# Performance work log

Measured on AMD Instinct MI355X. Metric: run time of the kernel, lower is better.

Reference implementation:

```python
import jax, jax.numpy as jnp
import numpy as np

B, N, T, CIN = 16, 400, 12, 2
HID, H, D = 256, 8, 32
P, EMB, TOPK, K = 3, 10, 16, 3


def _conv1d(x, w, b, dil):
    # x: (BN, C, T), w: (O, I, K); causal (left) padding like F.pad((pad,0))
    pad = (K - 1) * dil
    y = jax.lax.conv_general_dilated(x, w, (1,), [(pad, 0)], rhs_dilation=(dil,),
                                     dimension_numbers=('NCH', 'OIH', 'NCH'))
    return y + b[None, :, None]


def _ln(x, g, b):
    m = x.mean(-1, keepdims=True)
    v = x.var(-1, keepdims=True)
    return (x - m) / jnp.sqrt(v + 1e-5) * g + b


def setup_inputs() -> dict:
    key = jax.random.key(0)
    kit = iter(jax.random.split(key, 64))

    def g(shape, s=0.05):
        return jax.random.normal(next(kit), shape, jnp.float32) * s

    # fixed graph: ring with 8 neighbors + self loop -> L = 9*N edges
    idx = np.arange(N)
    offs = np.array([-4, -3, -2, -1, 0, 1, 2, 3, 4])
    recv = np.repeat(idx, offs.size)
    send = (recv + np.tile(offs, N)) % N
    L = recv.size

    inp = {
        'x': g((B, N, T, CIN), 1.0),
        'edge_feat': g((B, L, 2), 1.0),
        'fixed_edge_index': jnp.asarray(np.stack([recv, send]).astype(np.int32)),
        # GTCN layer 0 (dilation 1): gate/filter/skip convs + LayerNorm
        'wg0': g((HID, CIN, K)), 'bg0': jnp.zeros((HID,), jnp.float32),
        'wf0': g((HID, CIN, K)), 'bf0': jnp.zeros((HID,), jnp.float32),
        'ws0': g((HID, CIN, K)), 'bs0': jnp.zeros((HID,), jnp.float32),
        'ln0g': jnp.ones((HID,), jnp.float32), 'ln0b': jnp.zeros((HID,), jnp.float32),
        # GTCN layer 1 (dilation 2)
        'wg1': g((HID, HID, K)), 'bg1': jnp.zeros((HID,), jnp.float32),
        'wf1': g((HID, HID, K)), 'bf1': jnp.zeros((HID,), jnp.float32),
        'ws1': g((HID, HID, K)), 'bs1': jnp.zeros((HID,), jnp.float32),
        'ln1g': jnp.ones((HID,), jnp.float32), 'ln1b': jnp.zeros((HID,), jnp.float32),
        'wsk': g((CIN, HID)), 'bsk': jnp.zeros((HID,), jnp.float32),
        # sparse GAT on fixed physical graph (with 2-dim edge features)
        'sWq': g((HID, HID)), 'sWk': g((HID, HID)), 'sWv': g((HID, HID)),
        'sWe': g((2, HID)),
        'saq': g((H, D)), 'sak': g((H, D)), 'sae': g((H, D)),
        # dense GAT on adaptive adjacency
        'dWq': g((HID, HID)), 'dWk': g((HID, HID)), 'dWv': g((HID, HID)),
        'daq': g((H, D)), 'dak': g((H, D)),
        'E1': g((N, EMB), 0.5), 'E2': g((N, EMB), 0.5),
        # gated fusion
        'fW1': g((HID, HID)), 'fb1': jnp.zeros((HID,), jnp.float32),
        'fW2': g((HID, HID)), 'fb2': jnp.zeros((HID,), jnp.float32),
        'fW3': g((HID, HID)), 'fb3': jnp.zeros((HID,), jnp.float32),
        # prediction head
        'Wo': g((HID, P)), 'bo': jnp.zeros((P,), jnp.float32),
    }
    return inp


def reference(x, edge_feat,
              wg0, bg0, wf0, bf0, ws0, bs0, ln0g, ln0b,
              wg1, bg1, wf1, bf1, ws1, bs1, ln1g, ln1b, wsk, bsk,
              sWq, sWk, sWv, sWe, saq, sak, sae,
              dWq, dWk, dWv, daq, dak, E1, E2,
              fW1, fb1, fW2, fb2, fW3, fb3, Wo, bo,
              fixed_edge_index):
    Bb, Nn, Tt, _ = x.shape
    # ---- GTCN (gated temporal conv stack with residual skip) ----
    res = x @ wsk + bsk                                   # (B,N,T,HID)
    xc = x.reshape(Bb * Nn, Tt, -1).transpose(0, 2, 1)    # (BN,C,T)
    for (wg, bg, wf, bf, ws, bs, lg, lb), dil in (
            ((wg0, bg0, wf0, bf0, ws0, bs0, ln0g, ln0b), 1),
            ((wg1, bg1, wf1, bf1, ws1, bs1, ln1g, ln1b), 2)):
        gate = jax.nn.sigmoid(_conv1d(xc, wg, bg, dil))
        y = gate * _conv1d(xc, wf, bf, dil) + (1 - gate) * _conv1d(xc, ws, bs, dil)
        y = jax.nn.relu(_ln(y.transpose(0, 2, 1), lg, lb))  # (BN,T,HID)
        xc = y.transpose(0, 2, 1)
    h = xc.transpose(0, 2, 1).reshape(Bb, Nn, Tt, HID) + res
    hl = h[:, :, -1, :]                                   # (B,N,HID) last step

    # ---- sparse GAT on fixed physical graph (edge features) ----
    recv, send = fixed_edge_index[0], fixed_edge_index[1]
    q = (hl @ sWq).reshape(Bb, Nn, H, D)
    k = (hl @ sWk).reshape(Bb, Nn, H, D)
    v = (hl @ sWv).reshape(Bb, Nn, H, D)
    e = (edge_feat @ sWe).reshape(Bb, -1, H, D)
    s = (q[:, recv] * saq).sum(-1) + (k[:, send] * sak).sum(-1) + (e * sae).sum(-1)
    s = jax.nn.leaky_relu(s, 0.2)                         # (B,L,H)
    mx = jnp.full((Bb, Nn, H), -jnp.inf, s.dtype).at[:, recv].max(s)
    ex = jnp.exp(s - mx[:, recv])
    den = jnp.zeros((Bb, Nn, H), s.dtype).at[:, recv].add(ex)
    alpha = ex / jnp.clip(den[:, recv], 1e-12, None)
    agg = jnp.zeros((Bb, Nn, H, D), v.dtype).at[:, recv].add(alpha[..., None] * v[:, send])
    h_fixed = jax.nn.elu(agg.reshape(Bb, Nn, HID))

    # ---- dense GAT on adaptive (learned, top-k sparsified) adjacency ----
    A = jax.nn.softmax(jax.nn.relu(E1 @ E2.T), axis=-1)   # (N,N)
    kth = jax.lax.top_k(A, TOPK)[0][:, -1:]
    adj_adp = jnp.where(A >= kth, A, 0.0)
    q = (hl @ dWq).reshape(Bb, Nn, H, D)
    k = (hl @ dWk).reshape(Bb, Nn, H, D)
    v = (hl @ dWv).reshape(Bb, Nn, H, D)
    sc = (q * daq).sum(-1)[:, :, None, :] + (k * dak).sum(-1)[:, None, :, :]  # (B,N,N,H)
    sc = jax.nn.leaky_relu(sc, 0.2)
    sc = sc + jnp.log(jnp.clip(adj_adp, 1e-12, None))[None, :, :, None]      # log-adj trick
    sc = jnp.where((adj_adp > 0)[None, :, :, None], sc, -1e9)
    al = jax.nn.softmax(sc, axis=2)
    h_adp = jax.nn.elu(jnp.einsum('bnjh,bjhd->bnhd', al, v).reshape(Bb, Nn, HID))

    # ---- gated fusion + prediction head ----
    gate = jax.nn.sigmoid((h_fixed + h_adp) @ fW1 + fb1)
    fused = jnp.tanh(gate * (h_fixed @ fW2 + fb2) + (1 - gate) * (h_adp @ fW3 + fb3))
    return fused @ Wo + bo                                # (B,N,P)
```

## Files before the change

kernel.cpp:

```cpp
#include <hip/hip_runtime.h>
#include <math.h>

#define LL 3600
#define NODES 6400

typedef __attribute__((ext_vector_type(8))) _Float16 half8;
typedef __attribute__((ext_vector_type(4))) float f32x4;

__device__ __forceinline__ unsigned short f2h(float f) {
    union { _Float16 h; unsigned short u; } cv;
    cv.h = (_Float16)f;
    return cv.u;
}
__device__ __forceinline__ float h2f(unsigned short u) {
    union { unsigned short u; _Float16 h; } cv;
    cv.u = u;
    return (float)cv.h;
}

#define GLOAD16(gp, lp) __builtin_amdgcn_global_load_lds( \
    (const __attribute__((address_space(1))) unsigned int*)(const void*)(gp), \
    (__attribute__((address_space(3))) unsigned int*)(void*)(lp), 16, 0, 0)

__device__ __forceinline__ void block_reduce_sum2(float a, float b, float* red, float& ra, float& rb) {
    #pragma unroll
    for (int o = 32; o > 0; o >>= 1) { a += __shfl_xor(a, o, 64); b += __shfl_xor(b, o, 64); }
    int w = threadIdx.x >> 6, l = threadIdx.x & 63;
    if (l == 0) { red[w] = a; red[4 + w] = b; }
    __syncthreads();
    ra = red[0] + red[1] + red[2] + red[3];
    rb = red[4] + red[5] + red[6] + red[7];
    __syncthreads();
}

__global__ __launch_bounds__(256) void prep_kernel(
    const float* __restrict__ wg1, const float* __restrict__ wf1, const float* __restrict__ ws1,
    const float* __restrict__ sWv, const float* __restrict__ dWv,
    const float* __restrict__ sWq, const float* __restrict__ saq,
    const float* __restrict__ sWk, const float* __restrict__ sak,
    const float* __restrict__ dWq, const float* __restrict__ daq,
    const float* __restrict__ dWk, const float* __restrict__ dak,
    const float* __restrict__ fW1, const float* __restrict__ fW2, const float* __restrict__ fW3,
    const float* __restrict__ sWe, const float* __restrict__ sae,
    const float* __restrict__ E1, const float* __restrict__ E2,
    const float* __restrict__ x,
    const float* __restrict__ wg0, const float* __restrict__ bg0,
    const float* __restrict__ wf0, const float* __restrict__ bf0,
    const float* __restrict__ ws0, const float* __restrict__ bs0,
    const float* __restrict__ lg0, const float* __restrict__ lb0,
    unsigned short* __restrict__ W1h,
    unsigned short* __restrict__ W2h,
    unsigned short* __restrict__ W3h,
    float* __restrict__ AeS,
    int* __restrict__ cnt, int* __restrict__ idxs, float* __restrict__ logv,
    unsigned short* __restrict__ Xh) {
    __shared__ float smem[22];
    int bid = blockIdx.x;
    int tid = threadIdx.x;

    if (bid < 2304) {
        int idx = bid * 256 + tid;
        int n = idx / 768, k = idx % 768;
        int which = n >> 8, o = n & 255;
        int tt = k >> 8, i = k & 255;
        const float* w = which == 0 ? wg1 : (which == 1 ? wf1 : ws1);
        W1h[idx] = f2h(w[(o * 256 + i) * 3 + tt]);
    } else if (bid < 2944) {
        int idx = (bid - 2304) * 256 + tid;
        int n = idx / 256, k = idx % 256;
        float v = 0.f;
        if (n < 256) v = sWv[k * 256 + n];
        else if (n < 512) v = dWv[k * 256 + (n - 256)];
        else if (n < 544) {
            int j = n - 512, g = j >> 3, h = j & 7;
            const float* Wm = g == 0 ? sWq : (g == 1 ? sWk : (g == 2 ? dWq : dWk));
            const float* am = g == 0 ? saq : (g == 1 ? sak : (g == 2 ? daq : dak));
            float s = 0.f;
            for (int d = 0; d < 32; d++) s += Wm[k * 256 + h * 32 + d] * am[h * 32 + d];
            v = s;
        }
        W2h[idx] = f2h(v);
    } else if (bid < 4480) {
        int idx = (bid - 2944) * 256 + tid;
        int n = idx / 512, k = idx % 512;
        float v = 0.f;
        if (k < 256) {
            if (n < 256) v = fW1[k * 256 + n];
            else if (n < 512) v = fW2[k * 256 + (n - 256)];
        } else {
            int c = k - 256;
            if (n < 256) v = fW1[c * 256 + n];
            else if (n >= 512) v = fW3[c * 256 + (n - 512)];
        }
        W3h[idx] = f2h(v);
    } else if (bid == 4480) {
        if (tid < 16) {
            int cc = tid / 8, h = tid % 8;
            float s = 0.f;
            for (int d = 0; d < 32; d++) s += sWe[cc * 256 + h * 32 + d] * sae[h * 32 + d];
            AeS[tid] = s;
        }
    } else if (bid < 4581) {
        int n = ((bid - 4481) * 256 + tid) >> 6;
        int lane = tid & 63;
        if (n >= 400) return;
        float e1[10];
        #pragma unroll
        for (int k = 0; k < 10; k++) e1[k] = E1[n * 10 + k];
        float p[7];
        #pragma unroll
        for (int i = 0; i < 7; i++) {
            int j = i * 64 + lane;
            if (j < 400) {
                float s = 0.f;
                #pragma unroll
                for (int k = 0; k < 10; k++) s += e1[k] * E2[j * 10 + k];
                p[i] = fmaxf(s, 0.f);
            } else p[i] = -1e30f;
        }
        float mx = -1e30f;
        #pragma unroll
        for (int i = 0; i < 7; i++) mx = fmaxf(mx, p[i]);
        #pragma unroll
        for (int o = 32; o > 0; o >>= 1) mx = fmaxf(mx, __shfl_xor(mx, o, 64));
        float sum = 0.f;
        #pragma unroll
        for (int i = 0; i < 7; i++) {
            int j = i * 64 + lane;
            if (j < 400) { p[i] = expf(p[i] - mx); sum += p[i]; }
        }
        #pragma unroll
        for (int o = 32; o > 0; o >>= 1) sum += __shfl_xor(sum, o, 64);
        float inv = 1.f / sum;
        float m[7];
        #pragma unroll
        for (int i = 0; i < 7; i++) {
            int j = i * 64 + lane;
            if (j < 400) { p[i] *= inv; m[i] = p[i]; }
            else m[i] = -1e30f;
        }
        for (int it = 0; it < 15; ++it) {
            float lm = m[0];
            #pragma unroll
            for (int i = 1; i < 7; i++) lm = fmaxf(lm, m[i]);
            float gm = lm;
            #pragma unroll
            for (int o = 32; o > 0; o >>= 1) gm = fmaxf(gm, __shfl_xor(gm, o, 64));
            unsigned long long msk = __ballot(lm == gm);
            int first = (int)(__ffsll((long long)msk)) - 1;
            if (lane == first) {
                #pragma unroll
                for (int i = 0; i < 7; i++) {
                    if (m[i] == gm) { m[i] = -1e30f; break; }
                }
            }
        }
        float kth = m[0];
        #pragma unroll
        for (int i = 1; i < 7; i++) kth = fmaxf(kth, m[i]);
        #pragma unroll
        for (int o = 32; o > 0; o >>= 1) kth = fmaxf(kth, __shfl_xor(kth, o, 64));
        int base = 0;
        #pragma unroll
        for (int i = 0; i < 7; i++) {
            int j = i * 64 + lane;
            bool pred = (j < 400) && (p[i] >= kth);
            unsigned long long msk = __ballot(pred);
            int pre = __popcll(msk & ((lane == 63) ? 0x7fffffffffffffffull : ((1ull << lane) - 1)));
            if (pred) {
                int pos = base + pre;
                if (pos < 64) {
                    idxs[n * 64 + pos] = j;
                    logv[n * 64 + pos] = logf(fmaxf(p[i], 1e-12f));
                }
            }
            base += __popcll(msk);
        }
        if (lane == 0) cnt[n] = base < 64 ? base : 64;
    } else {
        int node = bid - 4581;
        int o = tid;
        float* xs = smem;
        float* red = smem + 14;
        if (o < 14) { int t = 5 + o / 2, c = o & 1; xs[(t - 5) * 2 + c] = x[(size_t)(node * 12 + t) * 2 + c]; }
        __syncthreads();
        float wg[6], wf[6], wsv[6];
        for (int i = 0; i < 6; i++) { wg[i] = wg0[o * 6 + i]; wf[i] = wf0[o * 6 + i]; wsv[i] = ws0[o * 6 + i]; }
        float bg = bg0[o], bf = bf0[o], bs = bs0[o];
        float gln = lg0[o], bln = lb0[o];
        for (int tt = 0; tt < 3; tt++) {
            int t = 7 + 2 * tt;
            float g = bg, f = bf, s = bs;
            for (int k = 0; k < 3; k++) {
                int ti = t - 2 + k - 5;
                for (int c = 0; c < 2; c++) {
                    float xv = xs[ti * 2 + c];
                    g += wg[c * 3 + k] * xv;
                    f += wf[c * 3 + k] * xv;
                    s += wsv[c * 3 + k] * xv;
                }
            }
            float gate = 1.f / (1.f + expf(-g));
            float y = gate * f + (1.f - gate) * s;
            float sum, sq;
            block_reduce_sum2(y, y * y, red, sum, sq);
            float mean = sum * (1.f / 256.f);
            float var = sq * (1.f / 256.f) - mean * mean;
            float v = (y - mean) * rsqrtf(var + 1e-5f) * gln + bln;
            v = fmaxf(v, 0.f);
            Xh[(size_t)node * 768 + tt * 256 + o] = f2h(v);
        }
    }
}

template<int K, int LDC, int GX>
__global__ __launch_bounds__(256, 4) void gemm_f16(
    const unsigned short* __restrict__ A,
    const unsigned short* __restrict__ BT,
    unsigned short* __restrict__ C) {
    __shared__ __align__(16) unsigned short lA[3][64 * 32];
    __shared__ __align__(16) unsigned short lB[3][64 * 32];
    int tid = threadIdx.x;
    int lane = tid & 63;
    int w = tid >> 6;
    int wm = w >> 1, wn = w & 1;
    int r = lane & 15, g4 = lane >> 4;

    constexpr int NWG = GX * 100;
    constexpr int Q = NWG / 8, R = NWG % 8;
    int flat = blockIdx.y * GX + blockIdx.x;
    int xcd = flat & 7, idx = flat >> 3;
    int nf = (xcd < R ? xcd * (Q + 1) : R * (Q + 1) + (xcd - R) * Q) + idx;
    int col0 = (nf % GX) * 64;
    int row0 = (nf / GX) * 64;

    f32x4 acc[2][2] = {};

    int rS = tid >> 2;
    int slot = tid & 3;
    int tk = (slot ^ (rS & 3)) * 8;

#define STAGE(sel, kk) do { \
    GLOAD16(A + (size_t)(row0 + rS) * K + (kk) + tk, &lA[sel][tid * 8]); \
    GLOAD16(BT + (size_t)(col0 + rS) * K + (kk) + tk, &lB[sel][tid * 8]); \
} while (0)

    int sw = (g4 ^ (r & 3)) << 3;

#define COMPUTE(cur) do { \
    half8 a_[2], b_[2]; \
    _Pragma("unroll") \
    for (int mi = 0; mi < 2; ++mi) \
        a_[mi] = *(const half8*)&lA[cur][(wm * 32 + mi * 16 + r) * 32 + sw]; \
    _Pragma("unroll") \
    for (int ni = 0; ni < 2; ++ni) \
        b_[ni] = *(const half8*)&lB[cur][(wn * 32 + ni * 16 + r) * 32 + sw]; \
    _Pragma("unroll") \
    for (int mi = 0; mi < 2; ++mi) \
        _Pragma("unroll") \
        for (int ni = 0; ni < 2; ++ni) \
            acc[mi][ni] = __builtin_amdgcn_mfma_f32_16x16x32_f16(a_[mi], b_[ni], acc[mi][ni], 0, 0, 0); \
} while (0)

    constexpr int NT = K >> 5;
    STAGE(0, 0);
    STAGE(1, 32);
    for (int t = 0; t < NT - 1; ++t) {
        asm volatile("s_waitcnt vmcnt(2)" ::: "memory");
        __builtin_amdgcn_s_barrier();
        if (t + 2 < NT) STAGE((t + 2) % 3, (t + 2) * 32);
        COMPUTE(t % 3);
    }
    asm volatile("s_waitcnt vmcnt(0)" ::: "memory");
    __builtin_amdgcn_s_barrier();
    COMPUTE((NT - 1) % 3);
#undef STAGE
#undef COMPUTE

    #pragma unroll
    for (int mi = 0; mi < 2; ++mi) {
        #pragma unroll
        for (int ni = 0; ni < 2; ++ni) {
            int rowb = row0 + wm * 32 + mi * 16 + g4 * 4;
            int colb = col0 + wn * 32 + ni * 16 + r;
            #pragma unroll
            for (int j = 0; j < 4; ++j)
                C[(size_t)(rowb + j) * LDC + colb] = f2h(acc[mi][ni][j]);
        }
    }
}

__global__ __launch_bounds__(256) void epi1_kernel(
    const unsigned short* __restrict__ Y1, const float* __restrict__ x,
    const float* __restrict__ bg1, const float* __restrict__ bf1, const float* __restrict__ bs1,
    const float* __restrict__ lg, const float* __restrict__ lb,
    const float* __restrict__ wsk, const float* __restrict__ bsk,
    unsigned short* __restrict__ HLh) {
    int node = blockIdx.x, o = threadIdx.x;
    __shared__ float red[8];
    size_t base = (size_t)node * 768;
    float g = h2f(Y1[base + o]) + bg1[o];
    float f = h2f(Y1[base + 256 + o]) + bf1[o];
    float s = h2f(Y1[base + 512 + o]) + bs1[o];
    float gate = 1.f / (1.f + expf(-g));
    float y = gate * f + (1.f - gate) * s;
    float sum, sq;
    block_reduce_sum2(y, y * y, red, sum, sq);
    float mean = sum * (1.f / 256.f);
    float var = sq * (1.f / 256.f) - mean * mean;
    float v = (y - mean) * rsqrtf(var + 1e-5f) * lg[o] + lb[o];
    v = fmaxf(v, 0.f);
    float x0 = x[(size_t)(node * 12 + 11) * 2];
    float x1 = x[(size_t)(node * 12 + 11) * 2 + 1];
    float res = x0 * wsk[o] + x1 * wsk[256 + o] + bsk[o];
    HLh[(size_t)node * 256 + o] = f2h(v + res);
}

__global__ __launch_bounds__(256) void gat_kernel(
    const unsigned short* __restrict__ Y2, const float* __restrict__ ef,
    const int* __restrict__ fei, const float* __restrict__ AeS,
    const int* __restrict__ cnt, const int* __restrict__ idxs, const float* __restrict__ logv,
    unsigned short* __restrict__ Uh) {
    int tid = threadIdx.x;
    if (blockIdx.x < NODES) {
        int node = blockIdx.x;
        int b = node / 400, n = node % 400;
        __shared__ int snd[9];
        __shared__ float sv[9][8];
        __shared__ float al[9][8];
        __shared__ float invden[8];
        if (tid < 9) snd[tid] = fei[LL + n * 9 + tid];
        __syncthreads();
        if (tid < 72) {
            int j = tid / 8, h = tid % 8;
            int l = n * 9 + j;
            float e0 = ef[((size_t)b * LL + l) * 2];
            float e1 = ef[((size_t)b * LL + l) * 2 + 1];
            float ae = e0 * AeS[h] + e1 * AeS[8 + h];
            float aq = h2f(Y2[(size_t)node * 640 + 512 + h]);
            float ak = h2f(Y2[((size_t)(b * 400 + snd[j])) * 640 + 520 + h]);
            float s = aq + ak + ae;
            s = s > 0.f ? s : 0.2f * s;
            sv[j][h] = s;
        }
        __syncthreads();
        if (tid < 8) {
            int h = tid;
            float mx = -1e30f;
            #pragma unroll
            for (int j = 0; j < 9; j++) mx = fmaxf(mx, sv[j][h]);
            float den = 0.f;
            #pragma unroll
            for (int j = 0; j < 9; j++) { float e = expf(sv[j][h] - mx); al[j][h] = e; den += e; }
            invden[h] = 1.f / fmaxf(den, 1e-12f);
        }
        __syncthreads();
        int h = tid >> 5;
        float acc = 0.f;
        #pragma unroll
        for (int j = 0; j < 9; j++)
            acc += al[j][h] * h2f(Y2[((size_t)(b * 400 + snd[j])) * 640 + tid]);
        acc *= invden[h];
        float e = acc > 0.f ? acc : (expf(acc) - 1.f);
        Uh[(size_t)node * 512 + tid] = f2h(e);
    } else {
        int node = blockIdx.x - NODES;
        int b = node / 400, n = node % 400;
        __shared__ int jidx[64];
        __shared__ float jlog[64];
        __shared__ float sc[64][8];
        __shared__ float alb[64][8];
        __shared__ float red8[8][8];
        __shared__ float mxd[8];
        __shared__ float invden[8];
        int c = cnt[n];
        if (tid < c) { jidx[tid] = idxs[n * 64 + tid]; jlog[tid] = logv[n * 64 + tid]; }
        __syncthreads();
        for (int e = tid; e < c * 8; e += 256) {
            int j = e / 8, h = e % 8;
            float aq = h2f(Y2[(size_t)node * 640 + 528 + h]);
            float ak = h2f(Y2[((size_t)(b * 400 + jidx[j])) * 640 + 536 + h]);
            float s = aq + ak;
            s = s > 0.f ? s : 0.2f * s;
            sc[j][h] = s + jlog[j];
        }
        __syncthreads();
        if (tid < 64) {
            int h = tid >> 3, grp = tid & 7;
            float mx = -1e30f;
            for (int j = grp; j < c; j += 8) mx = fmaxf(mx, sc[j][h]);
            red8[h][grp] = mx;
        }
        __syncthreads();
        if (tid < 8) {
            float mx = red8[tid][0];
            #pragma unroll
            for (int g = 1; g < 8; g++) mx = fmaxf(mx, red8[tid][g]);
            mxd[tid] = mx;
        }
        __syncthreads();
        if (tid < 64) {
            int h = tid >> 3, grp = tid & 7;
            float mx = mxd[h], s = 0.f;
            for (int j = grp; j < c; j += 8) { float e = expf(sc[j][h] - mx); alb[j][h] = e; s += e; }
            red8[h][grp] = s;
        }
        __syncthreads();
        if (tid < 8) {
            float s = 0.f;
            #pragma unroll
            for (int g = 0; g < 8; g++) s += red8[tid][g];
            invden[tid] = 1.f / s;
        }
        __syncthreads();
        int h = tid >> 5;
        float acc = 0.f;
        for (int j = 0; j < c; j++)
            acc += alb[j][h] * h2f(Y2[((size_t)(b * 400 + jidx[j])) * 640 + 256 + tid]);
        acc *= invden[h];
        float e = acc > 0.f ? acc : (expf(acc) - 1.f);
        Uh[(size_t)node * 512 + 256 + tid] = f2h(e);
    }
}

__global__ __launch_bounds__(256) void final_kernel(
    const unsigned short* __restrict__ Y3,
    const float* __restrict__ fb1, const float* __restrict__ fb2, const float* __restrict__ fb3,
    const float* __restrict__ Wo, const float* __restrict__ bo,
    float* __restrict__ out) {
    int node = blockIdx.x, o = threadIdx.x;
    __shared__ float red[12];
    size_t base = (size_t)node * 768;
    float g = 1.f / (1.f + expf(-(h2f(Y3[base + o]) + fb1[o])));
    float a2 = h2f(Y3[base + 256 + o]) + fb2[o];
    float a3 = h2f(Y3[base + 512 + o]) + fb3[o];
    float fused = tanhf(g * a2 + (1.f - g) * a3);
    float v0 = fused * Wo[o * 3 + 0];
    float v1 = fused * Wo[o * 3 + 1];
    float v2 = fused * Wo[o * 3 + 2];
    #pragma unroll
    for (int off = 32; off > 0; off >>= 1) {
        v0 += __shfl_xor(v0, off, 64);
        v1 += __shfl_xor(v1, off, 64);
        v2 += __shfl_xor(v2, off, 64);
    }
    int w = o >> 6, l = o & 63;
    if (l == 0) { red[w] = v0; red[4 + w] = v1; red[8 + w] = v2; }
    __syncthreads();
    if (o < 3) {
        float s = red[o * 4] + red[o * 4 + 1] + red[o * 4 + 2] + red[o * 4 + 3];
        out[(size_t)node * 3 + o] = s + bo[o];
    }
}

extern "C" void kernel_launch(void* const* d_in, const int* in_sizes, int n_in,
                              void* d_out, int out_size, void* d_ws, size_t ws_size,
                              hipStream_t stream) {
    const float* x   = (const float*)d_in[0];
    const float* ef  = (const float*)d_in[1];
    const int*   fei = (const int*)d_in[2];
    const float* wg0 = (const float*)d_in[3];
    const float* bg0 = (const float*)d_in[4];
    const float* wf0 = (const float*)d_in[5];
    const float* bf0 = (const float*)d_in[6];
    const float* ws0 = (const float*)d_in[7];
    const float* bs0 = (const float*)d_in[8];
    const float* ln0g = (const float*)d_in[9];
    const float* ln0b = (const float*)d_in[10];
    const float* wg1 = (const float*)d_in[11];
    const float* bg1 = (const float*)d_in[12];
    const float* wf1 = (const float*)d_in[13];
    const float* bf1 = (const float*)d_in[14];
    const float* ws1 = (const float*)d_in[15];
    const float* bs1 = (const float*)d_in[16];
    const float* ln1g = (const float*)d_in[17];
    const float* ln1b = (const float*)d_in[18];
    const float* wsk = (const float*)d_in[19];
    const float* bsk = (const float*)d_in[20];
    const float* sWq = (const float*)d_in[21];
    const float* sWk = (const float*)d_in[22];
    const float* sWv = (const float*)d_in[23];
    const float* sWe = (const float*)d_in[24];
    const float* saq = (const float*)d_in[25];
    const float* sak = (const float*)d_in[26];
    const float* sae = (const float*)d_in[27];
    const float* dWq = (const float*)d_in[28];
    const float* dWk = (const float*)d_in[29];
    const float* dWv = (const float*)d_in[30];
    const float* daq = (const float*)d_in[31];
    const float* dak = (const float*)d_in[32];
    const float* E1  = (const float*)d_in[33];
    const float* E2  = (const float*)d_in[34];
    const float* fW1 = (const float*)d_in[35];
    const float* fb1 = (const float*)d_in[36];
    const float* fW2 = (const float*)d_in[37];
    const float* fb2 = (const float*)d_in[38];
    const float* fW3 = (const float*)d_in[39];
    const float* fb3 = (const float*)d_in[40];
    const float* Wo  = (const float*)d_in[41];
    const float* bo  = (const float*)d_in[42];
    float* out = (float*)d_out;

    char* b = (char*)d_ws;
    unsigned short* Xh  = (unsigned short*)(b + 0);
    unsigned short* Yh  = (unsigned short*)(b + 9830400);
    unsigned short* HLh = (unsigned short*)(b + 19660800);
    unsigned short* Uh  = (unsigned short*)(b + 22937600);
    unsigned short* W1h = (unsigned short*)(b + 29491200);
    unsigned short* W2h = (unsigned short*)(b + 30670848);
    unsigned short* W3h = (unsigned short*)(b + 30998528);
    float*          AES = (float*)(b + 31784960);
    float*          LOGV= (float*)(b + 31785216);
    int*            CNT = (int*)(b + 31887616);
    int*            IDX = (int*)(b + 31889216);

    prep_kernel<<<10981, 256, 0, stream>>>(
        wg1, wf1, ws1,
        sWv, dWv, sWq, saq, sWk, sak, dWq, daq, dWk, dak,
        fW1, fW2, fW3, sWe, sae, E1, E2,
        x, wg0, bg0, wf0, bf0, ws0, bs0, ln0g, ln0b,
        W1h, W2h, W3h, AES,
        CNT, IDX, LOGV, Xh);

    gemm_f16<768, 768, 12><<<dim3(12, 100), 256, 0, stream>>>(Xh, W1h, Yh);

    epi1_kernel<<<NODES, 256, 0, stream>>>(Yh, x, bg1, bf1, bs1, ln1g, ln1b, wsk, bsk, HLh);

    gemm_f16<256, 640, 10><<<dim3(10, 100), 256, 0, stream>>>(HLh, W2h, Yh);

    gat_kernel<<<2 * NODES, 256, 0, stream>>>(Yh, ef, fei, AES, CNT, IDX, LOGV, Uh);

    gemm_f16<512, 768, 12><<<dim3(12, 100), 256, 0, stream>>>(Uh, W3h, Yh);

    final_kernel<<<NODES, 256, 0, stream>>>(Yh, fb1, fb2, fb3, Wo, bo, out);
}
```

Measured before the change: 108.6 us.

## Use wave-per-node layer-0 conv, merge GAT branches, raise GEMM occupancy

The layer-0 conv+LayerNorm section of prep_kernel now handles one node per wavefront with four channels per lane. Its reduction becomes a pure shuffle, so the shared-memory barriers go away, and results are written as packed 64-bit stores. The fixed-graph and adaptive GAT blocks are merged into one block per node: separate waves compute the two softmaxes, and the softmax reductions switch from shared-memory passes to shuffles. Aggregation reads two halves at once. The epi1 reduction drops its trailing barrier, and the GEMM launch bounds ask for 6 blocks per CU, which may cause register spills.

```diff
diff --git a/kernel.cpp b/kernel.cpp
--- a/kernel.cpp
+++ b/kernel.cpp
@@ -21,17 +21,6 @@
 #define GLOAD16(gp, lp) __builtin_amdgcn_global_load_lds( \
     (const __attribute__((address_space(1))) unsigned int*)(const void*)(gp), \
     (__attribute__((address_space(3))) unsigned int*)(void*)(lp), 16, 0, 0)
-
-__device__ __forceinline__ void block_reduce_sum2(float a, float b, float* red, float& ra, float& rb) {
-    #pragma unroll
-    for (int o = 32; o > 0; o >>= 1) { a += __shfl_xor(a, o, 64); b += __shfl_xor(b, o, 64); }
-    int w = threadIdx.x >> 6, l = threadIdx.x & 63;
-    if (l == 0) { red[w] = a; red[4 + w] = b; }
-    __syncthreads();
-    ra = red[0] + red[1] + red[2] + red[3];
-    rb = red[4] + red[5] + red[6] + red[7];
-    __syncthreads();
-}
 
 __global__ __launch_bounds__(256) void prep_kernel(
     const float* __restrict__ wg1, const float* __restrict__ wf1, const float* __restrict__ ws1,
@@ -54,7 +43,6 @@
     float* __restrict__ AeS,
     int* __restrict__ cnt, int* __restrict__ idxs, float* __restrict__ logv,
     unsigned short* __restrict__ Xh) {
-    __shared__ float smem[22];
     int bid = blockIdx.x;
     int tid = threadIdx.x;
 
@@ -178,43 +166,73 @@
         }
         if (lane == 0) cnt[n] = base < 64 ? base : 64;
     } else {
-        int node = bid - 4581;
-        int o = tid;
-        float* xs = smem;
-        float* red = smem + 14;
-        if (o < 14) { int t = 5 + o / 2, c = o & 1; xs[(t - 5) * 2 + c] = x[(size_t)(node * 12 + t) * 2 + c]; }
-        __syncthreads();
-        float wg[6], wf[6], wsv[6];
-        for (int i = 0; i < 6; i++) { wg[i] = wg0[o * 6 + i]; wf[i] = wf0[o * 6 + i]; wsv[i] = ws0[o * 6 + i]; }
-        float bg = bg0[o], bf = bf0[o], bs = bs0[o];
-        float gln = lg0[o], bln = lb0[o];
+        int lane = tid & 63;
+        int node = (bid - 4581) * 4 + (tid >> 6);
+        float xs[14];
+        #pragma unroll
+        for (int t = 0; t < 7; t++) {
+            xs[t * 2]     = x[(size_t)(node * 12 + 5 + t) * 2];
+            xs[t * 2 + 1] = x[(size_t)(node * 12 + 5 + t) * 2 + 1];
+        }
+        float wg[4][6], wf[4][6], wsv[4][6], bgv[4], bfv[4], bsv[4], gln[4], bln[4];
+        #pragma unroll
+        for (int cc = 0; cc < 4; cc++) {
+            int o = lane * 4 + cc;
+            #pragma unroll
+            for (int i = 0; i < 6; i++) {
+                wg[cc][i] = wg0[o * 6 + i];
+                wf[cc][i] = wf0[o * 6 + i];
+                wsv[cc][i] = ws0[o * 6 + i];
+            }
+            bgv[cc] = bg0[o]; bfv[cc] = bf0[o]; bsv[cc] = bs0[o];
+            gln[cc] = lg0[o]; bln[cc] = lb0[o];
+        }
+        #pragma unroll
         for (int tt = 0; tt < 3; tt++) {
-            int t = 7 + 2 * tt;
-            float g = bg, f = bf, s = bs;
-            for (int k = 0; k < 3; k++) {
-                int ti = t - 2 + k - 5;
-                for (int c = 0; c < 2; c++) {
-                    float xv = xs[ti * 2 + c];
-                    g += wg[c * 3 + k] * xv;
-                    f += wf[c * 3 + k] * xv;
-                    s += wsv[c * 3 + k] * xv;
+            int tb = 2 * tt;
+            float y[4];
+            float s1 = 0.f, s2 = 0.f;
+            #pragma unroll
+            for (int cc = 0; cc < 4; cc++) {
+                float g = bgv[cc], f = bfv[cc], s = bsv[cc];
+                #pragma unroll
+                for (int k = 0; k < 3; k++) {
+                    #pragma unroll
+                    for (int c = 0; c < 2; c++) {
+                        float xv = xs[(tb + k) * 2 + c];
+                        g += wg[cc][c * 3 + k] * xv;
+                        f += wf[cc][c * 3 + k] * xv;
+                        s += wsv[cc][c * 3 + k] * xv;
+                    }
                 }
+                float gate = 1.f / (1.f + expf(-g));
+                y[cc] = gate * f + (1.f - gate) * s;
+                s1 += y[cc];
+                s2 += y[cc] * y[cc];
             }
-            float gate = 1.f / (1.f + expf(-g));
-            float y = gate * f + (1.f - gate) * s;
-            float sum, sq;
-            block_reduce_sum2(y, y * y, red, sum, sq);
-            float mean = sum * (1.f / 256.f);
-            float var = sq * (1.f / 256.f) - mean * mean;
-            float v = (y - mean) * rsqrtf(var + 1e-5f) * gln + bln;
-            v = fmaxf(v, 0.f);
-            Xh[(size_t)node * 768 + tt * 256 + o] = f2h(v);
+            #pragma unroll
+            for (int o = 32; o > 0; o >>= 1) {
+                s1 += __shfl_xor(s1, o, 64);
+                s2 += __shfl_xor(s2, o, 64);
+            }
+            float mean = s1 * (1.f / 256.f);
+            float var = s2 * (1.f / 256.f) - mean * mean;
+            float rstd = rsqrtf(var + 1e-5f);
+            unsigned short h4[4];
+            #pragma unroll
+            for (int cc = 0; cc < 4; cc++) {
+                float v = (y[cc] - mean) * rstd * gln[cc] + bln[cc];
+                h4[cc] = f2h(fmaxf(v, 0.f));
+            }
+            unsigned long long pack = (unsigned long long)h4[0] | ((unsigned long long)h4[1] << 16)
+                                    | ((unsigned long long)h4[2] << 32) | ((unsigned long long)h4[3] << 48);
+            *(unsigned long long*)&Xh[(size_t)node * 768 + tt * 256 + lane * 4] = pack;
         }
     }
 }
 
 template<int K, int LDC, int GX>
-__global__ __launch_bounds__(256, 4) void gemm_f16(
+__global__ __launch_bounds__(256, 6) void gemm_f16(
     const unsigned short* __restrict__ A,
     const unsigned short* __restrict__ BT,
     unsigned short* __restrict__ C) {
@@ -304,8 +322,14 @@
     float s = h2f(Y1[base + 512 + o]) + bs1[o];
     float gate = 1.f / (1.f + expf(-g));
     float y = gate * f + (1.f - gate) * s;
-    float sum, sq;
-    block_reduce_sum2(y, y * y, red, sum, sq);
+    float a = y, bb = y * y;
+    #pragma unroll
+    for (int off = 32; off > 0; off >>= 1) { a += __shfl_xor(a, off, 64); bb += __shfl_xor(bb, off, 64); }
+    int w = o >> 6, l = o & 63;
+    if (l == 0) { red[w] = a; red[4 + w] = bb; }
+    __syncthreads();
+    float sum = red[0] + red[1] + red[2] + red[3];
+    float sq = red[4] + red[5] + red[6] + red[7];
     float mean = sum * (1.f / 256.f);
     float var = sq * (1.f / 256.f) - mean * mean;
     float v = (y - mean) * rsqrtf(var + 1e-5f) * lg[o] + lb[o];
@@ -321,18 +345,24 @@
     const int* __restrict__ fei, const float* __restrict__ AeS,
     const int* __restrict__ cnt, const int* __restrict__ idxs, const float* __restrict__ logv,
     unsigned short* __restrict__ Uh) {
+    int node = blockIdx.x;
+    int b = node / 400, n = node % 400;
     int tid = threadIdx.x;
-    if (blockIdx.x < NODES) {
-        int node = blockIdx.x;
-        int b = node / 400, n = node % 400;
-        __shared__ int snd[9];
-        __shared__ float sv[9][8];
-        __shared__ float al[9][8];
-        __shared__ float invden[8];
-        if (tid < 9) snd[tid] = fei[LL + n * 9 + tid];
-        __syncthreads();
-        if (tid < 72) {
-            int j = tid / 8, h = tid % 8;
+    __shared__ int snd[9];
+    __shared__ float alf[9][8];
+    __shared__ float invdf[8];
+    __shared__ int jidx[64];
+    __shared__ float sca[64][8];
+    __shared__ float alb[64][8];
+    __shared__ float invda[8];
+    __shared__ float svf[9][8];
+    int c = cnt[n];
+
+    if (tid < 64) {
+        int lane = tid;
+        if (lane < 9) snd[lane] = fei[LL + n * 9 + lane];
+        for (int e = lane; e < 72; e += 64) {
+            int j = e >> 3, h = e & 7;
             int l = n * 9 + j;
             float e0 = ef[((size_t)b * LL + l) * 2];
             float e1 = ef[((size_t)b * LL + l) * 2 + 1];
@@ -340,86 +370,76 @@
             float aq = h2f(Y2[(size_t)node * 640 + 512 + h]);
             float ak = h2f(Y2[((size_t)(b * 400 + snd[j])) * 640 + 520 + h]);
             float s = aq + ak + ae;
-            s = s > 0.f ? s : 0.2f * s;
-            sv[j][h] = s;
-        }
-        __syncthreads();
-        if (tid < 8) {
-            int h = tid;
+            svf[j][h] = s > 0.f ? s : 0.2f * s;
+        }
+        if (lane < 8) {
+            int h = lane;
             float mx = -1e30f;
             #pragma unroll
-            for (int j = 0; j < 9; j++) mx = fmaxf(mx, sv[j][h]);
+            for (int j = 0; j < 9; j++) mx = fmaxf(mx, svf[j][h]);
             float den = 0.f;
             #pragma unroll
-            for (int j = 0; j < 9; j++) { float e = expf(sv[j][h] - mx); al[j][h] = e; den += e; }
-            invden[h] = 1.f / fmaxf(den, 1e-12f);
-        }
-        __syncthreads();
-        int h = tid >> 5;
-        float acc = 0.f;
-        #pragma unroll
-        for (int j = 0; j < 9; j++)
-            acc += al[j][h] * h2f(Y2[((size_t)(b * 400 + snd[j])) * 640 + tid]);
-        acc *= invden[h];
-        float e = acc > 0.f ? acc : (expf(acc) - 1.f);
-        Uh[(size_t)node * 512 + tid] = f2h(e);
-    } else {
-        int node = blockIdx.x - NODES;
-        int b = node / 400, n = node % 400;
-        __shared__ int jidx[64];
-        __shared__ float jlog[64];
-        __shared__ float sc[64][8];
-        __shared__ float alb[64][8];
-        __shared__ float red8[8][8];
-        __shared__ float mxd[8];
-        __shared__ float invden[8];
-        int c = cnt[n];
-        if (tid < c) { jidx[tid] = idxs[n * 64 + tid]; jlog[tid] = logv[n * 64 + tid]; }
-        __syncthreads();
-        for (int e = tid; e < c * 8; e += 256) {
-            int j = e / 8, h = e % 8;
+            for (int j = 0; j < 9; j++) { float e = expf(svf[j][h] - mx); alf[j][h] = e; den += e; }
+            invdf[h] = 1.f / fmaxf(den, 1e-12f);
+        }
+    } else if (tid < 128) {
+        int lane = tid - 64;
+        if (lane < c) jidx[lane] = idxs[n * 64 + lane];
+        float jl = (lane < c) ? logv[n * 64 + lane] : 0.f;
+        for (int e = lane; e < c * 8; e += 64) {
+            int j = e >> 3, h = e & 7;
             float aq = h2f(Y2[(size_t)node * 640 + 528 + h]);
             float ak = h2f(Y2[((size_t)(b * 400 + jidx[j])) * 640 + 536 + h]);
             float s = aq + ak;
             s = s > 0.f ? s : 0.2f * s;
-            sc[j][h] = s + jlog[j];
-        }
-        __syncthreads();
-        if (tid < 64) {
-            int h = tid >> 3, grp = tid & 7;
-            float mx = -1e30f;
-            for (int j = grp; j < c; j += 8) mx = fmaxf(mx, sc[j][h]);
-            red8[h][grp] = mx;
-        }
-        __syncthreads();
-        if (tid < 8) {
-            float mx = red8[tid][0];
-            #pragma unroll
-            for (int g = 1; g < 8; g++) mx = fmaxf(mx, red8[tid][g]);
-            mxd[tid] = mx;
-        }
-        __syncthreads();
-        if (tid < 64) {
-            int h = tid >> 3, grp = tid & 7;
-            float mx = mxd[h], s = 0.f;
-            for (int j = grp; j < c; j += 8) { float e = expf(sc[j][h] - mx); alb[j][h] = e; s += e; }
-            red8[h][grp] = s;
-        }
-        __syncthreads();
-        if (tid < 8) {
-            float s = 0.f;
-            #pragma unroll
-            for (int g = 0; g < 8; g++) s += red8[tid][g];
-            invden[tid] = 1.f / s;
-        }
-        __syncthreads();
-        int h = tid >> 5;
-        float acc = 0.f;
-        for (int j = 0; j < c; j++)
-            acc += alb[j][h] * h2f(Y2[((size_t)(b * 400 + jidx[j])) * 640 + 256 + tid]);
-        acc *= invden[h];
-        float e = acc > 0.f ? acc : (expf(acc) - 1.f);
-        Uh[(size_t)node * 512 + 256 + tid] = f2h(e);
+            sca[j][h] = s + __shfl(jl, j, 64);
+        }
+        int h = lane >> 3, grp = lane & 7;
+        float mx = -1e30f;
+        for (int j = grp; j < c; j += 8) mx = fmaxf(mx, sca[j][h]);
+        #pragma unroll
+        for (int o = 1; o < 8; o <<= 1) mx = fmaxf(mx, __shfl_xor(mx, o, 64));
+        float s = 0.f;
+        for (int j = grp; j < c; j += 8) { float e = expf(sca[j][h] - mx); alb[j][h] = e; s += e; }
+        #pragma unroll
+        for (int o = 1; o < 8; o <<= 1) s += __shfl_xor(s, o, 64);
+        if (grp == 0) invda[h] = 1.f / s;
+    }
+    __syncthreads();
+
+    if (tid < 128) {
+        int ch = tid * 2;
+        int h = ch >> 5;
+        float a0 = 0.f, a1 = 0.f;
+        #pragma unroll
+        for (int j = 0; j < 9; j++) {
+            unsigned v = *(const unsigned*)&Y2[((size_t)(b * 400 + snd[j])) * 640 + ch];
+            float al = alf[j][h];
+            a0 += al * h2f((unsigned short)(v & 0xffff));
+            a1 += al * h2f((unsigned short)(v >> 16));
+        }
+        float iv = invdf[h];
+        a0 *= iv; a1 *= iv;
+        a0 = a0 > 0.f ? a0 : (expf(a0) - 1.f);
+        a1 = a1 > 0.f ? a1 : (expf(a1) - 1.f);
+        unsigned o = (unsigned)f2h(a0) | ((unsigned)f2h(a1) << 16);
+        *(unsigned*)&Uh[(size_t)node * 512 + ch] = o;
+    } else {
+        int ch = (tid - 128) * 2;
+        int h = ch >> 5;
+        float a0 = 0.f, a1 = 0.f;
+        for (int j = 0; j < c; j++) {
+            unsigned v = *(const unsigned*)&Y2[((size_t)(b * 400 + jidx[j])) * 640 + 256 + ch];
+            float al = alb[j][h];
+            a0 += al * h2f((unsigned short)(v & 0xffff));
+            a1 += al * h2f((unsigned short)(v >> 16));
+        }
+        float iv = invda[h];
+        a0 *= iv; a1 *= iv;
+        a0 = a0 > 0.f ? a0 : (expf(a0) - 1.f);
+        a1 = a1 > 0.f ? a1 : (expf(a1) - 1.f);
+        unsigned o = (unsigned)f2h(a0) | ((unsigned)f2h(a1) << 16);
+        *(unsigned*)&Uh[(size_t)node * 512 + 256 + ch] = o;
     }
 }
 
@@ -514,7 +534,7 @@
     int*            CNT = (int*)(b + 31887616);
     int*            IDX = (int*)(b + 31889216);
 
-    prep_kernel<<<10981, 256, 0, stream>>>(
+    prep_kernel<<<6181, 256, 0, stream>>>(
         wg1, wf1, ws1,
         sWv, dWv, sWq, saq, sWk, sak, dWq, daq, dWk, dak,
         fW1, fW2, fW3, sWe, sae, E1, E2,
@@ -528,7 +548,7 @@
 
     gemm_f16<256, 640, 10><<<dim3(10, 100), 256, 0, stream>>>(HLh, W2h, Yh);
 
-    gat_kernel<<<2 * NODES, 256, 0, stream>>>(Yh, ef, fei, AES, CNT, IDX, LOGV, Uh);
+    gat_kernel<<<NODES, 256, 0, stream>>>(Yh, ef, fei, AES, CNT, IDX, LOGV, Uh);
 
     gemm_f16<512, 768, 12><<<dim3(12, 100), 256, 0, stream>>>(Uh, W3h, Yh);
 
```

After: 100.1 us. 1.08x faster.
